# Performance work log

Hardware: AMD Instinct MI355X
Metric: run time of the kernel (lower is better)

Reference implementation:

```python
import jax, jax.numpy as jnp
import numpy as np

B, T, C = 4, 2048, 2048
N_HEAD = 16
HEAD_DIM = C // N_HEAD
ROPE_BASE = 10000.0


def setup_inputs() -> dict:
    key = jax.random.key(0)
    k1, k2, k3 = jax.random.split(key, 3)
    x = jax.random.normal(k1, (B, T, C), dtype=jnp.float32)
    Wqkv = jax.random.normal(k2, (C, 3 * C), dtype=jnp.float32) * 0.02
    bqkv = jnp.zeros((3 * C,), dtype=jnp.float32)
    Wproj = jax.random.normal(k3, (C, C), dtype=jnp.float32) * 0.02
    bproj = jnp.zeros((C,), dtype=jnp.float32)
    return {"x": x, "Wqkv": Wqkv, "bqkv": bqkv, "Wproj": Wproj, "bproj": bproj}


def _rope_cos_sin(seq_len, head_dim, dtype):
    inv_freq = 1.0 / (ROPE_BASE ** (jnp.arange(0, head_dim, 2, dtype=jnp.float32) / head_dim))
    t = jnp.arange(seq_len, dtype=jnp.float32)
    freqs = jnp.einsum("i,j->ij", t, inv_freq)          # [T, D/2]
    emb = jnp.concatenate([freqs, freqs], axis=-1)       # [T, D]
    return jnp.cos(emb).astype(dtype), jnp.sin(emb).astype(dtype)


def _rotate_half(x):
    half = x.shape[-1] // 2
    x1, x2 = x[..., :half], x[..., half:]
    return jnp.concatenate([-x2, x1], axis=-1)


def reference(x, Wqkv, bqkv, Wproj, bproj):
    b, t, c = x.shape
    qkv = x @ Wqkv + bqkv                                # [B, T, 3C]
    q, k, v = jnp.split(qkv, 3, axis=-1)
    # [B, T, C] -> [B, H, T, D]
    def to_heads(u):
        return u.reshape(b, t, N_HEAD, HEAD_DIM).transpose(0, 2, 1, 3)
    q, k, v = to_heads(q), to_heads(k), to_heads(v)
    cos, sin = _rope_cos_sin(t, HEAD_DIM, x.dtype)       # [T, D]
    cos = cos[None, None]                                # [1, 1, T, D]
    sin = sin[None, None]
    q = q * cos + _rotate_half(q) * sin
    k = k * cos + _rotate_half(k) * sin
    scale = 1.0 / np.sqrt(HEAD_DIM).astype(np.float32)
    scores = jnp.einsum("bhqd,bhkd->bhqk", q, k) * scale  # [B, H, T, T]
    causal = jnp.tril(jnp.ones((t, t), dtype=bool))
    scores = jnp.where(causal[None, None], scores, jnp.finfo(scores.dtype).min)
    att = jax.nn.softmax(scores, axis=-1)
    y = jnp.einsum("bhqk,bhkd->bhqd", att, v)             # [B, H, T, D]
    y = y.transpose(0, 2, 1, 3).reshape(b, t, c)
    return y @ Wproj + bproj
```

## Files before the change

kernel.cpp:

```cpp
#include <hip/hip_runtime.h>
#include <hip/hip_bf16.h>
#include <stdint.h>
#include <math.h>

#define NB 4
#define NT 2048
#define NC 2048
#define NH 16
#define HD 128
#define BT (NB*NT)

typedef __attribute__((ext_vector_type(8))) short s16x8;
typedef __attribute__((ext_vector_type(4))) short s16x4;
typedef __attribute__((ext_vector_type(4))) float f32x4;

typedef __attribute__((address_space(1))) void as1_void;
typedef __attribute__((address_space(3))) void as3_void;

static __device__ __forceinline__ unsigned short f2bf(float f) {
  union { float f; uint32_t u; } v; v.f = f;
  return (unsigned short)((v.u + 0x7fffu + ((v.u >> 16) & 1u)) >> 16);
}
static __device__ __forceinline__ float bf2f(unsigned short u) {
  union { uint32_t u; float f; } v; v.u = ((uint32_t)u) << 16;
  return v.f;
}
static __device__ __forceinline__ void async16(unsigned short* lds, const unsigned short* g) {
  __builtin_amdgcn_global_load_lds((as1_void*)g, (as3_void*)lds, 16, 0, 0);
}
static __device__ __forceinline__ uint32_t lds_off(void* p) {
  return (uint32_t)(size_t)(as3_void*)p;
}

__global__ void k_prep(const float* __restrict__ x, unsigned short* __restrict__ xb,
                       const float* __restrict__ Wqkv, unsigned short* __restrict__ WqkvT,
                       const float* __restrict__ Wproj, unsigned short* __restrict__ WprojT) {
  __shared__ unsigned short tile[64][65];
  const int blk = blockIdx.x;
  const int t = threadIdx.x;
  if (blk < 8192) {
    const int i = blk * 256 + t;
    const float4* p = (const float4*)x + (size_t)i * 2;
    float4 a = p[0], b = p[1];
    union { unsigned short s[8]; uint4 u; } o;
    o.s[0] = f2bf(a.x); o.s[1] = f2bf(a.y); o.s[2] = f2bf(a.z); o.s[3] = f2bf(a.w);
    o.s[4] = f2bf(b.x); o.s[5] = f2bf(b.y); o.s[6] = f2bf(b.z); o.s[7] = f2bf(b.w);
    ((uint4*)xb)[i] = o.u;
    return;
  }
  const float* W;
  unsigned short* WT;
  int bx, by, N;
  if (blk < 8192 + 3072) {
    const int id = blk - 8192;
    W = Wqkv; WT = WqkvT; N = 3 * NC; bx = id % 96; by = id / 96;
  } else {
    const int id = blk - 11264;
    W = Wproj; WT = WprojT; N = NC; bx = id % 32; by = id / 32;
  }
  const int K = NC;
  const int k0 = by * 64, n0 = bx * 64;
  const int jj = t & 63, base_i = t >> 6;
  #pragma unroll
  for (int p = 0; p < 16; ++p) {
    int i = p * 4 + base_i;
    tile[i][jj] = f2bf(W[(size_t)(k0 + i) * N + n0 + jj]);
  }
  __syncthreads();
  #pragma unroll
  for (int p = 0; p < 16; ++p) {
    int j = p * 4 + base_i;
    WT[(size_t)(n0 + j) * K + k0 + jj] = tile[jj][j];
  }
}

template<int MODE>
__global__ __launch_bounds__(256, 2)
void k_gemm_bt2(const unsigned short* __restrict__ A,
                const unsigned short* __restrict__ Bt,
                const float* __restrict__ bias,
                float* __restrict__ OutF,
                unsigned short* __restrict__ Qd,
                unsigned short* __restrict__ Kd,
                unsigned short* __restrict__ Vd,
                int M, int N, int K)
{
  __shared__ __align__(16) unsigned short Al[256 * 64];
  __shared__ __align__(16) unsigned short Bl[128 * 64];
  const int t = threadIdx.x;
  const int l = t & 63;
  const int wv = t >> 6;
  const int wm = wv >> 1, wn = wv & 1;
  const int bm = blockIdx.y * 256, bn = blockIdx.x * 128;
  const int lr = l & 15, lg = l >> 4;

  f32x4 acc[8][4];
  #pragma unroll
  for (int i = 0; i < 8; ++i)
    #pragma unroll
    for (int j = 0; j < 4; ++j)
      acc[i][j] = f32x4{0.f, 0.f, 0.f, 0.f};

  for (int k0 = 0; k0 < K; k0 += 64) {
    #pragma unroll
    for (int i = 0; i < 8; ++i) {
      const int Cc = i * 256 + t;
      const int row = Cc >> 3;
      const int kc = (Cc & 7) ^ (row & 7);
      async16(&Al[(i * 256 + (t & 192)) * 8], &A[(size_t)(bm + row) * K + k0 + kc * 8]);
    }
    #pragma unroll
    for (int i = 0; i < 4; ++i) {
      const int Cc = i * 256 + t;
      const int row = Cc >> 3;
      const int kc = (Cc & 7) ^ (row & 7);
      async16(&Bl[(i * 256 + (t & 192)) * 8], &Bt[(size_t)(bn + row) * K + k0 + kc * 8]);
    }
    __syncthreads();
    #pragma unroll
    for (int kk = 0; kk < 2; ++kk) {
      s16x8 af[8], bfr[4];
      #pragma unroll
      for (int mi = 0; mi < 8; ++mi) {
        const int row = wm * 128 + mi * 16 + lr;
        const int ch = (kk * 4 + lg) ^ (row & 7);
        af[mi] = *(const s16x8*)&Al[row * 64 + ch * 8];
      }
      #pragma unroll
      for (int ni = 0; ni < 4; ++ni) {
        const int row = wn * 64 + ni * 16 + lr;
        const int ch = (kk * 4 + lg) ^ (row & 7);
        bfr[ni] = *(const s16x8*)&Bl[row * 64 + ch * 8];
      }
      __builtin_amdgcn_s_setprio(1);
      #pragma unroll
      for (int mi = 0; mi < 8; ++mi)
        #pragma unroll
        for (int ni = 0; ni < 4; ++ni)
          acc[mi][ni] = __builtin_amdgcn_mfma_f32_16x16x32_bf16(af[mi], bfr[ni], acc[mi][ni], 0, 0, 0);
      __builtin_amdgcn_s_setprio(0);
    }
    __syncthreads();
  }

  if (MODE == 1) {
    #pragma unroll
    for (int mi = 0; mi < 8; ++mi) {
      #pragma unroll
      for (int ni = 0; ni < 4; ++ni) {
        const int col = bn + wn * 64 + ni * 16 + lr;
        const float bv = bias[col];
        #pragma unroll
        for (int r = 0; r < 4; ++r) {
          const int row = bm + wm * 128 + mi * 16 + lg * 4 + r;
          OutF[(size_t)row * N + col] = acc[mi][ni][r] + bv;
        }
      }
    }
  } else {
    const int whichB = bn >> 11;
    const int bb = bm >> 11;
    const int h = (bn & 2047) >> 7;
    unsigned short* dst = (whichB == 0) ? Qd : (whichB == 1 ? Kd : Vd);
    if (whichB == 2) {
      #pragma unroll
      for (int mi = 0; mi < 8; ++mi) {
        #pragma unroll
        for (int ni = 0; ni < 4; ++ni) {
          const int col = bn + wn * 64 + ni * 16 + lr;
          const float bv = bias[col];
          const int d = wn * 64 + ni * 16 + lr;
          #pragma unroll
          for (int r = 0; r < 4; ++r) {
            const int tp = (bm + wm * 128 + mi * 16 + lg * 4 + r) & 2047;
            dst[(((size_t)(bb * NH + h)) * NT + tp) * HD + d] = f2bf(acc[mi][ni][r] + bv);
          }
        }
      }
    } else {
      const float qsc = (whichB == 0) ? (0.08838834764831845f * 1.4426950408889634f) : 1.0f;
      float invf[4], crot[4], srot[4];
      #pragma unroll
      for (int ni = 0; ni < 4; ++ni) {
        invf[ni] = exp2f(-(float)(ni * 16 + lr) * 0.2076205059304602f);
        __sincosf(invf[ni], &srot[ni], &crot[ni]);
      }
      float* Ex = (float*)Al;
      #pragma unroll
      for (int mc = 0; mc < 4; ++mc) {
        __syncthreads();
        #pragma unroll
        for (int dm = 0; dm < 2; ++dm)
          #pragma unroll
          for (int ni = 0; ni < 4; ++ni) {
            const float bv = bias[bn + wn * 64 + ni * 16 + lr];
            #pragma unroll
            for (int r = 0; r < 4; ++r)
              Ex[(dm * 16 + ni * 4 + r) * 256 + wv * 64 + l] = acc[mc * 2 + dm][ni][r] + bv;
          }
        __syncthreads();
        #pragma unroll
        for (int dm = 0; dm < 2; ++dm) {
          const int mi = mc * 2 + dm;
          const int tpb = (bm + wm * 128 + mi * 16 + lg * 4) & 2047;
          #pragma unroll
          for (int ni = 0; ni < 4; ++ni) {
            const float bv = bias[bn + wn * 64 + ni * 16 + lr];
            const int d = wn * 64 + ni * 16 + lr;
            float s, c;
            __sincosf((float)tpb * invf[ni], &s, &c);
            #pragma unroll
            for (int r = 0; r < 4; ++r) {
              const int tp = tpb + r;
              const float own = acc[mi][ni][r] + bv;
              const float oth = Ex[(dm * 16 + ni * 4 + r) * 256 + (wv ^ 1) * 64 + l];
              const float out = ((wn == 0) ? (own * c - oth * s) : (own * c + oth * s)) * qsc;
              dst[(((size_t)(bb * NH + h)) * NT + tp) * HD + d] = f2bf(out);
              const float cn = c * crot[ni] - s * srot[ni];
              s = s * crot[ni] + c * srot[ni];
              c = cn;
            }
          }
        }
      }
    }
  }
}

__global__ __launch_bounds__(256, 2)
void k_attn(const unsigned short* __restrict__ Q,
            const unsigned short* __restrict__ Kg,
            const unsigned short* __restrict__ Vg,
            unsigned short* __restrict__ Yatt)
{
  __shared__ __align__(16) unsigned short Kl[2][64 * 128];
  __shared__ __align__(16) unsigned short Vl[2][64 * 128];
  const int bh = blockIdx.x;
  const int pair = blockIdx.y;
  const int b = bh >> 4, h = bh & 15;
  const int t = threadIdx.x, l = t & 63, wv = t >> 6;
  const int lr = l & 15, lg = l >> 4;
  const size_t hoff = (size_t)bh * NT * HD;
  const unsigned short* Qh = Q + hoff;
  const unsigned short* Kh = Kg + hoff;
  const unsigned short* Vh = Vg + hoff;
  const uint32_t vbase0 = lds_off(&Vl[0][0]);

  auto stageKV = [&](int buf, int kv0) {
    #pragma unroll
    for (int i = 0; i < 4; ++i) {
      const int Cc = i * 256 + t;
      {
        const int krow = Cc >> 4;
        const int kc = (Cc & 15) ^ (krow & 7);
        async16(&Kl[buf][(i * 256 + (t & 192)) * 8], &Kh[(size_t)(kv0 + krow) * HD + kc * 8]);
      }
      {
        const int S = Cc >> 3, c8 = Cc & 7;
        const int kq = S >> 3, dq = S & 7;
        const int vk = kq * 4 + (c8 >> 1), vd = dq * 16 + (c8 & 1) * 8;
        async16(&Vl[buf][(i * 256 + (t & 192)) * 8], &Vh[(size_t)(kv0 + vk) * HD + vd]);
      }
    }
  };

  #pragma unroll 1
  for (int rep = 0; rep < 2; ++rep) {
    const int qb16 = rep ? (15 - pair) : pair;
    const int q0w = qb16 * 128 + wv * 32;
    const int qrowA = q0w + lr, qrowB = q0w + 16 + lr;

    __syncthreads();

    s16x8 qfA[4], qfB[4];
    #pragma unroll
    for (int m = 0; m < 4; ++m) {
      qfA[m] = *(const s16x8*)(Qh + (size_t)qrowA * HD + m * 32 + lg * 8);
      qfB[m] = *(const s16x8*)(Qh + (size_t)qrowB * HD + m * 32 + lg * 8);
    }

    f32x4 ytA[8], ytB[8];
    #pragma unroll
    for (int n = 0; n < 8; ++n) { ytA[n] = f32x4{0.f,0.f,0.f,0.f}; ytB[n] = f32x4{0.f,0.f,0.f,0.f}; }
    float mrunA = -1e30f, lrunA = 0.f, mrunB = -1e30f, lrunB = 0.f;

    auto computeTile = [&](int buf, int kv0) {
      f32x4 stA[4], stB[4];
      __builtin_amdgcn_s_setprio(1);
      #pragma unroll
      for (int kt = 0; kt < 4; ++kt) {
        f32x4 a = f32x4{0.f,0.f,0.f,0.f}, bq = f32x4{0.f,0.f,0.f,0.f};
        const int krow = kt * 16 + lr;
        #pragma unroll
        for (int m = 0; m < 4; ++m) {
          const int ch = (m * 4 + lg) ^ (krow & 7);
          s16x8 kf = *(const s16x8*)&Kl[buf][krow * 128 + ch * 8];
          a  = __builtin_amdgcn_mfma_f32_16x16x32_bf16(kf, qfA[m], a, 0, 0, 0);
          bq = __builtin_amdgcn_mfma_f32_16x16x32_bf16(kf, qfB[m], bq, 0, 0, 0);
        }
        stA[kt] = a; stB[kt] = bq;
      }
      __builtin_amdgcn_s_setprio(0);

      if (kv0 + 63 > q0w) {
        #pragma unroll
        for (int kt = 0; kt < 4; ++kt)
          #pragma unroll
          for (int r = 0; r < 4; ++r) {
            const int key = kv0 + kt * 16 + lg * 4 + r;
            if (key > qrowA) stA[kt][r] = -3.0e38f;
            if (key > qrowB) stB[kt][r] = -3.0e38f;
          }
      }

      float tmA = -3.0e38f, tmB = -3.0e38f;
      #pragma unroll
      for (int kt = 0; kt < 4; ++kt)
        #pragma unroll
        for (int r = 0; r < 4; ++r) { tmA = fmaxf(tmA, stA[kt][r]); tmB = fmaxf(tmB, stB[kt][r]); }
      tmA = fmaxf(tmA, __shfl_xor(tmA, 16)); tmA = fmaxf(tmA, __shfl_xor(tmA, 32));
      tmB = fmaxf(tmB, __shfl_xor(tmB, 16)); tmB = fmaxf(tmB, __shfl_xor(tmB, 32));
      if (!__all((tmA - mrunA <= 8.0f) && (tmB - mrunB <= 8.0f))) {
        const float mnA = fmaxf(mrunA, tmA), mnB = fmaxf(mrunB, tmB);
        const float fsA = exp2f(mrunA - mnA), fsB = exp2f(mrunB - mnB);
        mrunA = mnA; mrunB = mnB;
        lrunA *= fsA; lrunB *= fsB;
        #pragma unroll
        for (int n = 0; n < 8; ++n)
          #pragma unroll
          for (int r = 0; r < 4; ++r) { ytA[n][r] *= fsA; ytB[n][r] *= fsB; }
      }

      float pvA[16], pvB[16];
      float psA = 0.f, psB = 0.f;
      #pragma unroll
      for (int kt = 0; kt < 4; ++kt)
        #pragma unroll
        for (int r = 0; r < 4; ++r) {
          const float pa = exp2f(stA[kt][r] - mrunA);
          const float pb = exp2f(stB[kt][r] - mrunB);
          psA += pa; psB += pb;
          pvA[kt * 4 + r] = pa; pvB[kt * 4 + r] = pb;
        }
      lrunA += psA; lrunB += psB;

      union { uint32_t w[4]; s16x8 v; } puA[2], puB[2];
      #pragma unroll
      for (int gk = 0; gk < 2; ++gk)
        #pragma unroll
        for (int w = 0; w < 4; ++w) {
          const int i0 = (gk * 2 + (w >> 1)) * 4 + (w & 1) * 2;
          asm("v_cvt_pk_bf16_f32 %0, %1, %2" : "=v"(puA[gk].w[w]) : "v"(pvA[i0]), "v"(pvA[i0 + 1]));
          asm("v_cvt_pk_bf16_f32 %0, %1, %2" : "=v"(puB[gk].w[w]) : "v"(pvB[i0]), "v"(pvB[i0 + 1]));
        }

      const uint32_t vb = vbase0 + (uint32_t)buf * 16384;
      #pragma unroll
      for (int gk = 0; gk < 2; ++gk) {
        s16x4 va[8], vb2[8];
        #pragma unroll
        for (int n = 0; n < 8; ++n) {
          const uint32_t a0 = vb + ((uint32_t)((gk * 8 + lg) * 8 + n)) * 128 + (uint32_t)lr * 8;
          asm volatile("ds_read_b64_tr_b16 %0, %1" : "=v"(va[n])  : "v"(a0));
          asm volatile("ds_read_b64_tr_b16 %0, %1" : "=v"(vb2[n]) : "v"(a0 + 4096));
        }
        asm volatile("s_waitcnt lgkmcnt(0)" ::: "memory");
        __builtin_amdgcn_sched_barrier(0);
        __builtin_amdgcn_s_setprio(1);
        #pragma unroll
        for (int n = 0; n < 8; ++n) {
          s16x8 vf;
          vf[0] = va[n][0];  vf[1] = va[n][1];  vf[2] = va[n][2];  vf[3] = va[n][3];
          vf[4] = vb2[n][0]; vf[5] = vb2[n][1]; vf[6] = vb2[n][2]; vf[7] = vb2[n][3];
          ytA[n] = __builtin_amdgcn_mfma_f32_16x16x32_bf16(vf, puA[gk].v, ytA[n], 0, 0, 0);
          ytB[n] = __builtin_amdgcn_mfma_f32_16x16x32_bf16(vf, puB[gk].v, ytB[n], 0, 0, 0);
        }
        __builtin_amdgcn_s_setprio(0);
      }
    };

    const int nkv = 2 * qb16 + 2;
    stageKV(0, 0);
    asm volatile("s_waitcnt vmcnt(0)" ::: "memory");
    __syncthreads();
    int buf = 0;
    #pragma unroll 1
    for (int kv = 0; kv < nkv - 1; ++kv) {
      stageKV(buf ^ 1, (kv + 1) * 64);
      computeTile(buf, kv * 64);
      asm volatile("s_waitcnt vmcnt(0)" ::: "memory");
      __builtin_amdgcn_s_barrier();
      buf ^= 1;
    }
    if ((nkv - 1) * 64 <= q0w + 31)
      computeTile(buf, (nkv - 1) * 64);

    lrunA += __shfl_xor(lrunA, 16); lrunA += __shfl_xor(lrunA, 32);
    lrunB += __shfl_xor(lrunB, 16); lrunB += __shfl_xor(lrunB, 32);
    const float invA = 1.f / lrunA, invB = 1.f / lrunB;
    unsigned short* yrowA = Yatt + (size_t)(b * NT + qrowA) * NC + h * HD;
    unsigned short* yrowB = Yatt + (size_t)(b * NT + qrowB) * NC + h * HD;
    #pragma unroll
    for (int n = 0; n < 8; ++n) {
      uint32_t u0, u1;
      asm("v_cvt_pk_bf16_f32 %0, %1, %2" : "=v"(u0) : "v"(ytA[n][0] * invA), "v"(ytA[n][1] * invA));
      asm("v_cvt_pk_bf16_f32 %0, %1, %2" : "=v"(u1) : "v"(ytA[n][2] * invA), "v"(ytA[n][3] * invA));
      uint2 pk; pk.x = u0; pk.y = u1;
      *(uint2*)(yrowA + n * 16 + lg * 4) = pk;
      asm("v_cvt_pk_bf16_f32 %0, %1, %2" : "=v"(u0) : "v"(ytB[n][0] * invB), "v"(ytB[n][1] * invB));
      asm("v_cvt_pk_bf16_f32 %0, %1, %2" : "=v"(u1) : "v"(ytB[n][2] * invB), "v"(ytB[n][3] * invB));
      pk.x = u0; pk.y = u1;
      *(uint2*)(yrowB + n * 16 + lg * 4) = pk;
    }
  }
}

extern "C" void kernel_launch(void* const* d_in, const int* in_sizes, int n_in,
                              void* d_out, int out_size, void* d_ws, size_t ws_size,
                              hipStream_t stream) {
  (void)in_sizes; (void)n_in; (void)out_size; (void)ws_size;
  const float* x     = (const float*)d_in[0];
  const float* Wqkv  = (const float*)d_in[1];
  const float* bqkv  = (const float*)d_in[2];
  const float* Wproj = (const float*)d_in[3];
  const float* bproj = (const float*)d_in[4];
  float* out = (float*)d_out;
  char* ws = (char*)d_ws;

  unsigned short* xb     = (unsigned short*)(ws);
  unsigned short* WqkvT  = (unsigned short*)(ws + 33554432);
  unsigned short* WprojT = (unsigned short*)(ws + 58720256);
  unsigned short* Qb     = (unsigned short*)(ws + 67108864);
  unsigned short* Kb     = (unsigned short*)(ws + 100663296);
  unsigned short* Vb     = (unsigned short*)(ws + 134217728);
  unsigned short* att    = xb;

  k_prep<<<dim3(12288), dim3(256), 0, stream>>>(x, xb, Wqkv, WqkvT, Wproj, WprojT);
  k_gemm_bt2<0><<<dim3(48, 32), dim3(256), 0, stream>>>(xb, WqkvT, bqkv, nullptr, Qb, Kb, Vb, BT, 3 * NC, NC);
  k_attn<<<dim3(64, 8), dim3(256), 0, stream>>>(Qb, Kb, Vb, att);
  k_gemm_bt2<1><<<dim3(16, 32), dim3(256), 0, stream>>>(att, WprojT, bproj, out, nullptr, nullptr, nullptr, BT, NC, NC);
}
```

Before: 399.6 us.

## Reshape GEMM wave tiling to 64x128 so RoPE pairs stay in-register

Changes the per-wave tile in the QKV/proj GEMM from 128x64 (2x2 wave grid) to 64x128 (4x1 wave grid), so each wave holds both halves of a head dimension. This lets the RoPE epilogue combine the low and high halves directly from registers, dropping the shared-memory exchange and its barriers. The trade-off is that each wave now loads 4 A fragments and 8 B fragments per k-step instead of 8 and 4, which keeps the LDS read volume roughly the same but shifts the reuse pattern.

```diff
diff --git a/kernel.cpp b/kernel.cpp
--- a/kernel.cpp
+++ b/kernel.cpp
@@ -89,16 +89,15 @@
   __shared__ __align__(16) unsigned short Bl[128 * 64];
   const int t = threadIdx.x;
   const int l = t & 63;
-  const int wv = t >> 6;
-  const int wm = wv >> 1, wn = wv & 1;
+  const int wm = t >> 6;
   const int bm = blockIdx.y * 256, bn = blockIdx.x * 128;
   const int lr = l & 15, lg = l >> 4;
 
-  f32x4 acc[8][4];
+  f32x4 acc[4][8];
   #pragma unroll
-  for (int i = 0; i < 8; ++i)
-    #pragma unroll
-    for (int j = 0; j < 4; ++j)
+  for (int i = 0; i < 4; ++i)
+    #pragma unroll
+    for (int j = 0; j < 8; ++j)
       acc[i][j] = f32x4{0.f, 0.f, 0.f, 0.f};
 
   for (int k0 = 0; k0 < K; k0 += 64) {
@@ -119,24 +118,24 @@
     __syncthreads();
     #pragma unroll
     for (int kk = 0; kk < 2; ++kk) {
-      s16x8 af[8], bfr[4];
-      #pragma unroll
-      for (int mi = 0; mi < 8; ++mi) {
-        const int row = wm * 128 + mi * 16 + lr;
+      s16x8 af[4], bfr[8];
+      #pragma unroll
+      for (int mi = 0; mi < 4; ++mi) {
+        const int row = wm * 64 + mi * 16 + lr;
         const int ch = (kk * 4 + lg) ^ (row & 7);
         af[mi] = *(const s16x8*)&Al[row * 64 + ch * 8];
       }
       #pragma unroll
-      for (int ni = 0; ni < 4; ++ni) {
-        const int row = wn * 64 + ni * 16 + lr;
+      for (int ni = 0; ni < 8; ++ni) {
+        const int row = ni * 16 + lr;
         const int ch = (kk * 4 + lg) ^ (row & 7);
         bfr[ni] = *(const s16x8*)&Bl[row * 64 + ch * 8];
       }
       __builtin_amdgcn_s_setprio(1);
       #pragma unroll
-      for (int mi = 0; mi < 8; ++mi)
-        #pragma unroll
-        for (int ni = 0; ni < 4; ++ni)
+      for (int mi = 0; mi < 4; ++mi)
+        #pragma unroll
+        for (int ni = 0; ni < 8; ++ni)
           acc[mi][ni] = __builtin_amdgcn_mfma_f32_16x16x32_bf16(af[mi], bfr[ni], acc[mi][ni], 0, 0, 0);
       __builtin_amdgcn_s_setprio(0);
     }
@@ -145,14 +144,14 @@
 
   if (MODE == 1) {
     #pragma unroll
-    for (int mi = 0; mi < 8; ++mi) {
-      #pragma unroll
-      for (int ni = 0; ni < 4; ++ni) {
-        const int col = bn + wn * 64 + ni * 16 + lr;
+    for (int mi = 0; mi < 4; ++mi) {
+      #pragma unroll
+      for (int ni = 0; ni < 8; ++ni) {
+        const int col = bn + ni * 16 + lr;
         const float bv = bias[col];
         #pragma unroll
         for (int r = 0; r < 4; ++r) {
-          const int row = bm + wm * 128 + mi * 16 + lg * 4 + r;
+          const int row = bm + wm * 64 + mi * 16 + lg * 4 + r;
           OutF[(size_t)row * N + col] = acc[mi][ni][r] + bv;
         }
       }
@@ -164,15 +163,14 @@
     unsigned short* dst = (whichB == 0) ? Qd : (whichB == 1 ? Kd : Vd);
     if (whichB == 2) {
       #pragma unroll
-      for (int mi = 0; mi < 8; ++mi) {
-        #pragma unroll
-        for (int ni = 0; ni < 4; ++ni) {
-          const int col = bn + wn * 64 + ni * 16 + lr;
-          const float bv = bias[col];
-          const int d = wn * 64 + ni * 16 + lr;
+      for (int mi = 0; mi < 4; ++mi) {
+        #pragma unroll
+        for (int ni = 0; ni < 8; ++ni) {
+          const float bv = bias[bn + ni * 16 + lr];
+          const int d = ni * 16 + lr;
           #pragma unroll
           for (int r = 0; r < 4; ++r) {
-            const int tp = (bm + wm * 128 + mi * 16 + lg * 4 + r) & 2047;
+            const int tp = (bm + wm * 64 + mi * 16 + lg * 4 + r) & 2047;
             dst[(((size_t)(bb * NH + h)) * NT + tp) * HD + d] = f2bf(acc[mi][ni][r] + bv);
           }
         }
@@ -185,41 +183,27 @@
         invf[ni] = exp2f(-(float)(ni * 16 + lr) * 0.2076205059304602f);
         __sincosf(invf[ni], &srot[ni], &crot[ni]);
       }
-      float* Ex = (float*)Al;
-      #pragma unroll
-      for (int mc = 0; mc < 4; ++mc) {
-        __syncthreads();
-        #pragma unroll
-        for (int dm = 0; dm < 2; ++dm)
+      #pragma unroll
+      for (int mi = 0; mi < 4; ++mi) {
+        const int tpb = (bm + wm * 64 + mi * 16 + lg * 4) & 2047;
+        #pragma unroll
+        for (int ni = 0; ni < 4; ++ni) {
+          const int dlo = ni * 16 + lr;
+          const float bvlo = bias[bn + dlo];
+          const float bvhi = bias[bn + dlo + 64];
+          float s, c;
+          __sincosf((float)tpb * invf[ni], &s, &c);
           #pragma unroll
-          for (int ni = 0; ni < 4; ++ni) {
-            const float bv = bias[bn + wn * 64 + ni * 16 + lr];
-            #pragma unroll
-            for (int r = 0; r < 4; ++r)
-              Ex[(dm * 16 + ni * 4 + r) * 256 + wv * 64 + l] = acc[mc * 2 + dm][ni][r] + bv;
-          }
-        __syncthreads();
-        #pragma unroll
-        for (int dm = 0; dm < 2; ++dm) {
-          const int mi = mc * 2 + dm;
-          const int tpb = (bm + wm * 128 + mi * 16 + lg * 4) & 2047;
-          #pragma unroll
-          for (int ni = 0; ni < 4; ++ni) {
-            const float bv = bias[bn + wn * 64 + ni * 16 + lr];
-            const int d = wn * 64 + ni * 16 + lr;
-            float s, c;
-            __sincosf((float)tpb * invf[ni], &s, &c);
-            #pragma unroll
-            for (int r = 0; r < 4; ++r) {
-              const int tp = tpb + r;
-              const float own = acc[mi][ni][r] + bv;
-              const float oth = Ex[(dm * 16 + ni * 4 + r) * 256 + (wv ^ 1) * 64 + l];
-              const float out = ((wn == 0) ? (own * c - oth * s) : (own * c + oth * s)) * qsc;
-              dst[(((size_t)(bb * NH + h)) * NT + tp) * HD + d] = f2bf(out);
-              const float cn = c * crot[ni] - s * srot[ni];
-              s = s * crot[ni] + c * srot[ni];
-              c = cn;
-            }
+          for (int r = 0; r < 4; ++r) {
+            const int tp = tpb + r;
+            const float lo = acc[mi][ni][r] + bvlo;
+            const float hi = acc[mi][ni + 4][r] + bvhi;
+            const size_t base = (((size_t)(bb * NH + h)) * NT + tp) * HD;
+            dst[base + dlo]      = f2bf((lo * c - hi * s) * qsc);
+            dst[base + dlo + 64] = f2bf((hi * c + lo * s) * qsc);
+            const float cn = c * crot[ni] - s * srot[ni];
+            s = s * crot[ni] + c * srot[ni];
+            c = cn;
           }
         }
       }
```

Measured after the change: 392.3 us. Within noise of the previous version (-1.8%).
